# Kernel tuning notes

Hardware: AMD Instinct MI355X
Metric: run time of the kernel (lower is better)

The kernel has to match this reference:

```python
import jax, jax.numpy as jnp
import numpy as np

NUM_VALUES = 1048576   # rows in the source value store
NUM_WEIGHTS = 65536    # unique learned weight matrices (deduplicated)
E = 4194304            # total (neuron, input) edges across the layer
DIN = 8
DOUT = 8


def setup_inputs() -> dict:
    key = jax.random.key(0)
    k1, k2, k3, k4 = jax.random.split(key, 4)
    values = jax.random.normal(k1, (NUM_VALUES, DIN), dtype=jnp.float32)
    weights = jax.random.normal(k2, (NUM_WEIGHTS, DOUT, DIN), dtype=jnp.float32)
    input_idx = jax.random.randint(k3, (E,), 0, NUM_VALUES, dtype=jnp.int32)
    weight_idx = jax.random.randint(k4, (E,), 0, NUM_WEIGHTS, dtype=jnp.int32)
    return {"values": values, "weights": weights,
            "input_idx": input_idx, "weight_idx": weight_idx}


def reference(values, weights, input_idx, weight_idx):
    # self.gather(layer_values): gather activations by precomputed ordinals
    x = jnp.take(values, input_idx, axis=0)          # [E, DIN]
    # self.gather_weights(w): gather (possibly shared) weight matrices
    w = jnp.take(weights, weight_idx, axis=0)        # [E, DOUT, DIN]
    # y = w @ input_values  (per-edge dense matmul)
    y = jnp.einsum('eoi,ei->eo', w, x)               # [E, DOUT]
    return y
```

## Files before the change

kernel.cpp:

```cpp
#include <hip/hip_runtime.h>
#include <hip/hip_bf16.h>
#include <stdint.h>


__device__ __forceinline__ float bflo(uint32_t u) {
    union { uint32_t u; float f; } c; c.u = u << 16; return c.f;
}
__device__ __forceinline__ float bfhi(uint32_t u) {
    union { uint32_t u; float f; } c; c.u = u & 0xffff0000u; return c.f;
}

__global__ __launch_bounds__(256) void convert_weights_kernel(
    const float4* __restrict__ src,
    ushort4*      __restrict__ dst,
    int n4)
{
    int i = blockIdx.x * blockDim.x + threadIdx.x;
    if (i >= n4) return;
    float4 v = src[i];
    ushort4 r;
    r.x = __bfloat16_as_ushort(__float2bfloat16(v.x));
    r.y = __bfloat16_as_ushort(__float2bfloat16(v.y));
    r.z = __bfloat16_as_ushort(__float2bfloat16(v.z));
    r.w = __bfloat16_as_ushort(__float2bfloat16(v.w));
    dst[i] = r;
}

__global__ __launch_bounds__(256) void edge_linear_bf16w_kernel(
    const float*    __restrict__ values,
    const uint32_t* __restrict__ wbf,
    const int*      __restrict__ input_idx,
    const int*      __restrict__ weight_idx,
    float*          __restrict__ out,
    int E)
{
    int gid = blockIdx.x * blockDim.x + threadIdx.x;
    int e = gid >> 3;
    if (e >= E) return;
    int o = gid & 7;

    int iidx = input_idx[e];
    int widx = weight_idx[e];

    const float4* xp = (const float4*)(values + (size_t)iidx * 8u);
    const uint4*  wp = (const uint4*)(wbf + (size_t)widx * 32u + (uint32_t)o * 4u);

    uint4  wv = *wp;
    float4 x0 = xp[0];
    float4 x1 = xp[1];

    float acc = 0.0f;
    acc = fmaf(bflo(wv.x), x0.x, acc);
    acc = fmaf(bfhi(wv.x), x0.y, acc);
    acc = fmaf(bflo(wv.y), x0.z, acc);
    acc = fmaf(bfhi(wv.y), x0.w, acc);
    acc = fmaf(bflo(wv.z), x1.x, acc);
    acc = fmaf(bfhi(wv.z), x1.y, acc);
    acc = fmaf(bflo(wv.w), x1.z, acc);
    acc = fmaf(bfhi(wv.w), x1.w, acc);

    out[gid] = acc;
}

__global__ __launch_bounds__(256) void edge_linear_f32_kernel(
    const float* __restrict__ values,
    const float* __restrict__ weights,
    const int*   __restrict__ input_idx,
    const int*   __restrict__ weight_idx,
    float*       __restrict__ out,
    int E)
{
    int gid = blockIdx.x * blockDim.x + threadIdx.x;
    int e = gid >> 3;
    if (e >= E) return;
    int o = gid & 7;
    int iidx = input_idx[e];
    int widx = weight_idx[e];
    const float4* xp = (const float4*)(values  + (size_t)iidx * 8u);
    const float4* wp = (const float4*)(weights + (size_t)widx * 64u + (uint32_t)o * 8u);
    float4 x0 = xp[0], x1 = xp[1], w0 = wp[0], w1 = wp[1];
    float acc = 0.0f;
    acc = fmaf(w0.x, x0.x, acc); acc = fmaf(w0.y, x0.y, acc);
    acc = fmaf(w0.z, x0.z, acc); acc = fmaf(w0.w, x0.w, acc);
    acc = fmaf(w1.x, x1.x, acc); acc = fmaf(w1.y, x1.y, acc);
    acc = fmaf(w1.z, x1.z, acc); acc = fmaf(w1.w, x1.w, acc);
    out[gid] = acc;
}

extern "C" void kernel_launch(void* const* d_in, const int* in_sizes, int n_in,
                              void* d_out, int out_size, void* d_ws, size_t ws_size,
                              hipStream_t stream) {
    const float* values     = (const float*)d_in[0];
    const float* weights    = (const float*)d_in[1];
    const int*   input_idx  = (const int*)d_in[2];
    const int*   weight_idx = (const int*)d_in[3];
    float*       out        = (float*)d_out;

    int E  = in_sizes[2];
    int NW = in_sizes[1];
    size_t need = (size_t)NW * sizeof(uint16_t);

    long long threads = (long long)E * 8;
    int block = 256;
    int grid = (int)((threads + block - 1) / block);

    if (ws_size >= need) {
        int n4 = NW / 4;
        int cgrid = (n4 + 255) / 256;
        convert_weights_kernel<<<cgrid, 256, 0, stream>>>(
            (const float4*)weights, (ushort4*)d_ws, n4);
        edge_linear_bf16w_kernel<<<grid, block, 0, stream>>>(
            values, (const uint32_t*)d_ws, input_idx, weight_idx, out, E);
    } else {
        edge_linear_f32_kernel<<<grid, block, 0, stream>>>(
            values, weights, input_idx, weight_idx, out, E);
    }
}
```

Baseline: 314.5 us.

## Counting-sort edges by weight index before per-edge matmul

Adds a histogram, a single-block scan and an atomic scatter that bucket the edges by weight index, then runs the per-edge matmul over the sorted order with fp32 weights and scatters each result back to its original edge slot. The aim is to make weight reads cache-friendly by grouping edges that share a weight matrix. In exchange it adds four kernels with heavy atomics, a serial one-block scan, extra index arrays in the workspace, and non-coalesced output writes. The bf16 weight path becomes a fallback used only when the workspace is too small.

```diff
diff --git a/kernel.cpp b/kernel.cpp
--- a/kernel.cpp
+++ b/kernel.cpp
@@ -1,6 +1,91 @@
 #include <hip/hip_runtime.h>
 #include <hip/hip_bf16.h>
 #include <stdint.h>
+
+
+#define NBINS 65536
+
+
+__global__ __launch_bounds__(256) void zero_bins_kernel(uint32_t* __restrict__ bins) {
+    int i = blockIdx.x * blockDim.x + threadIdx.x;
+    if (i < NBINS) bins[i] = 0u;
+}
+
+__global__ __launch_bounds__(256) void hist_kernel(
+    const int* __restrict__ weight_idx, uint32_t* __restrict__ bins, int E) {
+    int e = blockIdx.x * blockDim.x + threadIdx.x;
+    if (e < E) atomicAdd(&bins[(uint32_t)weight_idx[e]], 1u);
+}
+
+__global__ __launch_bounds__(1024) void scan_kernel(uint32_t* __restrict__ bins) {
+    __shared__ uint32_t sdata[1024];
+    int t = threadIdx.x;
+    uint32_t local[64];
+    uint32_t sum = 0;
+    int base_i = t * 64;
+#pragma unroll
+    for (int k = 0; k < 64; ++k) { local[k] = bins[base_i + k]; sum += local[k]; }
+    sdata[t] = sum;
+    __syncthreads();
+    for (int off = 1; off < 1024; off <<= 1) {
+        uint32_t v = (t >= off) ? sdata[t - off] : 0u;
+        __syncthreads();
+        sdata[t] += v;
+        __syncthreads();
+    }
+    uint32_t run = sdata[t] - sum;
+#pragma unroll
+    for (int k = 0; k < 64; ++k) { bins[base_i + k] = run; run += local[k]; }
+}
+
+__global__ __launch_bounds__(256) void scatter_kernel(
+    const int* __restrict__ input_idx, const int* __restrict__ weight_idx,
+    uint32_t* __restrict__ bins,
+    uint32_t* __restrict__ s_iidx, uint32_t* __restrict__ s_widx,
+    uint32_t* __restrict__ s_eid, int E) {
+    int e = blockIdx.x * blockDim.x + threadIdx.x;
+    if (e >= E) return;
+    uint32_t w = (uint32_t)weight_idx[e];
+    uint32_t i = (uint32_t)input_idx[e];
+    uint32_t pos = atomicAdd(&bins[w], 1u);
+    s_iidx[pos] = i;
+    s_widx[pos] = w;
+    s_eid[pos]  = (uint32_t)e;
+}
+
+
+__global__ __launch_bounds__(256) void edge_linear_sorted_kernel(
+    const float*    __restrict__ values,
+    const float*    __restrict__ weights,
+    const uint32_t* __restrict__ s_iidx,
+    const uint32_t* __restrict__ s_widx,
+    const uint32_t* __restrict__ s_eid,
+    float*          __restrict__ out,
+    int E)
+{
+    int gid = blockIdx.x * blockDim.x + threadIdx.x;
+    int j = gid >> 3;
+    if (j >= E) return;
+    int o = gid & 7;
+
+    uint32_t iidx = s_iidx[j];
+    uint32_t widx = s_widx[j];
+    uint32_t eid  = s_eid[j];
+
+    const float4* xp = (const float4*)(values  + (size_t)iidx * 8u);
+    const float4* wp = (const float4*)(weights + (size_t)widx * 64u + (uint32_t)o * 8u);
+
+    float4 x0 = xp[0], x1 = xp[1];
+    float4 w0 = wp[0], w1 = wp[1];
+
+    float acc = 0.0f;
+    acc = fmaf(w0.x, x0.x, acc); acc = fmaf(w0.y, x0.y, acc);
+    acc = fmaf(w0.z, x0.z, acc); acc = fmaf(w0.w, x0.w, acc);
+    acc = fmaf(w1.x, x1.x, acc); acc = fmaf(w1.y, x1.y, acc);
+    acc = fmaf(w1.z, x1.z, acc); acc = fmaf(w1.w, x1.w, acc);
+
+    out[(size_t)eid * 8u + (uint32_t)o] = acc;
+}
 
 
 __device__ __forceinline__ float bflo(uint32_t u) {
@@ -11,10 +96,7 @@
 }
 
 __global__ __launch_bounds__(256) void convert_weights_kernel(
-    const float4* __restrict__ src,
-    ushort4*      __restrict__ dst,
-    int n4)
-{
+    const float4* __restrict__ src, ushort4* __restrict__ dst, int n4) {
     int i = blockIdx.x * blockDim.x + threadIdx.x;
     if (i >= n4) return;
     float4 v = src[i];
@@ -27,49 +109,31 @@
 }
 
 __global__ __launch_bounds__(256) void edge_linear_bf16w_kernel(
-    const float*    __restrict__ values,
-    const uint32_t* __restrict__ wbf,
-    const int*      __restrict__ input_idx,
-    const int*      __restrict__ weight_idx,
-    float*          __restrict__ out,
-    int E)
-{
+    const float* __restrict__ values, const uint32_t* __restrict__ wbf,
+    const int* __restrict__ input_idx, const int* __restrict__ weight_idx,
+    float* __restrict__ out, int E) {
     int gid = blockIdx.x * blockDim.x + threadIdx.x;
     int e = gid >> 3;
     if (e >= E) return;
     int o = gid & 7;
-
     int iidx = input_idx[e];
     int widx = weight_idx[e];
-
     const float4* xp = (const float4*)(values + (size_t)iidx * 8u);
     const uint4*  wp = (const uint4*)(wbf + (size_t)widx * 32u + (uint32_t)o * 4u);
-
-    uint4  wv = *wp;
-    float4 x0 = xp[0];
-    float4 x1 = xp[1];
-
+    uint4 wv = *wp;
+    float4 x0 = xp[0], x1 = xp[1];
     float acc = 0.0f;
-    acc = fmaf(bflo(wv.x), x0.x, acc);
-    acc = fmaf(bfhi(wv.x), x0.y, acc);
-    acc = fmaf(bflo(wv.y), x0.z, acc);
-    acc = fmaf(bfhi(wv.y), x0.w, acc);
-    acc = fmaf(bflo(wv.z), x1.x, acc);
-    acc = fmaf(bfhi(wv.z), x1.y, acc);
-    acc = fmaf(bflo(wv.w), x1.z, acc);
-    acc = fmaf(bfhi(wv.w), x1.w, acc);
-
+    acc = fmaf(bflo(wv.x), x0.x, acc); acc = fmaf(bfhi(wv.x), x0.y, acc);
+    acc = fmaf(bflo(wv.y), x0.z, acc); acc = fmaf(bfhi(wv.y), x0.w, acc);
+    acc = fmaf(bflo(wv.z), x1.x, acc); acc = fmaf(bfhi(wv.z), x1.y, acc);
+    acc = fmaf(bflo(wv.w), x1.z, acc); acc = fmaf(bfhi(wv.w), x1.w, acc);
     out[gid] = acc;
 }
 
 __global__ __launch_bounds__(256) void edge_linear_f32_kernel(
-    const float* __restrict__ values,
-    const float* __restrict__ weights,
-    const int*   __restrict__ input_idx,
-    const int*   __restrict__ weight_idx,
-    float*       __restrict__ out,
-    int E)
-{
+    const float* __restrict__ values, const float* __restrict__ weights,
+    const int* __restrict__ input_idx, const int* __restrict__ weight_idx,
+    float* __restrict__ out, int E) {
     int gid = blockIdx.x * blockDim.x + threadIdx.x;
     int e = gid >> 3;
     if (e >= E) return;
@@ -87,6 +151,7 @@
     out[gid] = acc;
 }
 
+
 extern "C" void kernel_launch(void* const* d_in, const int* in_sizes, int n_in,
                               void* d_out, int out_size, void* d_ws, size_t ws_size,
                               hipStream_t stream) {
@@ -98,21 +163,37 @@
 
     int E  = in_sizes[2];
     int NW = in_sizes[1];
-    size_t need = (size_t)NW * sizeof(uint16_t);
 
-    long long threads = (long long)E * 8;
+    size_t bins_bytes = (size_t)NBINS * 4u;
+    size_t arr_bytes  = (size_t)E * 4u;
+    size_t need_sort  = bins_bytes + 3u * arr_bytes;
+
+    long long threads8 = (long long)E * 8;
     int block = 256;
-    int grid = (int)((threads + block - 1) / block);
+    int grid8 = (int)((threads8 + block - 1) / block);
+    int gridE = (E + block - 1) / block;
 
-    if (ws_size >= need) {
+    if (ws_size >= need_sort) {
+        uint32_t* bins   = (uint32_t*)d_ws;
+        uint32_t* s_iidx = (uint32_t*)((char*)d_ws + bins_bytes);
+        uint32_t* s_widx = (uint32_t*)((char*)d_ws + bins_bytes + arr_bytes);
+        uint32_t* s_eid  = (uint32_t*)((char*)d_ws + bins_bytes + 2u * arr_bytes);
+
+        zero_bins_kernel<<<NBINS / 256, 256, 0, stream>>>(bins);
+        hist_kernel<<<gridE, 256, 0, stream>>>(weight_idx, bins, E);
+        scan_kernel<<<1, 1024, 0, stream>>>(bins);
+        scatter_kernel<<<gridE, 256, 0, stream>>>(input_idx, weight_idx, bins,
+                                                  s_iidx, s_widx, s_eid, E);
+        edge_linear_sorted_kernel<<<grid8, block, 0, stream>>>(
+            values, weights, s_iidx, s_widx, s_eid, out, E);
+    } else if (ws_size >= (size_t)NW * 2u) {
         int n4 = NW / 4;
-        int cgrid = (n4 + 255) / 256;
-        convert_weights_kernel<<<cgrid, 256, 0, stream>>>(
+        convert_weights_kernel<<<(n4 + 255) / 256, 256, 0, stream>>>(
             (const float4*)weights, (ushort4*)d_ws, n4);
-        edge_linear_bf16w_kernel<<<grid, block, 0, stream>>>(
+        edge_linear_bf16w_kernel<<<grid8, block, 0, stream>>>(
             values, (const uint32_t*)d_ws, input_idx, weight_idx, out, E);
     } else {
-        edge_linear_f32_kernel<<<grid, block, 0, stream>>>(
+        edge_linear_f32_kernel<<<grid8, block, 0, stream>>>(
             values, weights, input_idx, weight_idx, out, E);
     }
 }
```

Measured after the change: 774.4 us. 2.46x slower.
